# Optimization experiments

Measured on AMD Instinct MI355X. Metric: run time of the kernel, lower is better.

## Reference

```python
import jax, jax.numpy as jnp
import numpy as np
from jax import lax

DEPTH, DIM, HEADS, DHEAD = 4, 384, 8, 64
INNER = HEADS * DHEAD          # 512
HID = int(DIM * 0.25)          # 96 (hardcoded in Transformer_Conv)
B, Hg, Wg = 8, 32, 32
N = Hg * Wg
SCALE = DHEAD ** -0.5
EPS = 1e-5


def _layer_norm(x, w, b):
    mu = jnp.mean(x, axis=-1, keepdims=True)
    var = jnp.mean(jnp.square(x - mu), axis=-1, keepdims=True)
    return (x - mu) * lax.rsqrt(var + EPS) * w + b


def setup_inputs() -> dict:
    key = jax.random.key(0)
    ks = jax.random.split(key, 8)
    s = 0.02
    return {
        "x": jax.random.normal(ks[0], (B, N, DIM), jnp.float32),
        "ln1_w": jnp.ones((DEPTH, DIM), jnp.float32),
        "ln1_b": jnp.zeros((DEPTH, DIM), jnp.float32),
        "w_qkv": jax.random.normal(ks[1], (DEPTH, DIM, 3 * INNER), jnp.float32) * s,
        "w_out": jax.random.normal(ks[2], (DEPTH, INNER, DIM), jnp.float32) * s,
        "b_out": jnp.zeros((DEPTH, DIM), jnp.float32),
        "ln2_w": jnp.ones((DEPTH, DIM), jnp.float32),
        "ln2_b": jnp.zeros((DEPTH, DIM), jnp.float32),
        "fc1_w": jax.random.normal(ks[3], (DEPTH, DIM, HID), jnp.float32) * s,
        "fc1_b": jnp.zeros((DEPTH, HID), jnp.float32),
        "dw_w": jax.random.normal(ks[4], (DEPTH, HID, 1, 3, 3), jnp.float32) * s,
        "dw_b": jnp.zeros((DEPTH, HID), jnp.float32),
        "fc2_w": jax.random.normal(ks[5], (DEPTH, HID, DIM), jnp.float32) * s,
        "fc2_b": jnp.zeros((DEPTH, DIM), jnp.float32),
        "H": Hg,
        "W": Wg,
    }


def _forward(x, ln1_w, ln1_b, w_qkv, w_out, b_out, ln2_w, ln2_b,
             fc1_w, fc1_b, dw_w, dw_b, fc2_w, fc2_b, H, W):
    b, n, c = x.shape
    attn_last = None
    for l in range(DEPTH):
        # ---- PreNorm + Attention (with post-softmax cross-layer residual) ----
        xn = _layer_norm(x, ln1_w[l], ln1_b[l])
        qkv = xn @ w_qkv[l]                                   # [b, n, 3*inner]
        q, k, v = jnp.split(qkv, 3, axis=-1)
        q = q.reshape(b, n, HEADS, DHEAD).transpose(0, 2, 1, 3)  # bhnd
        k = k.reshape(b, n, HEADS, DHEAD).transpose(0, 2, 1, 3)
        v = v.reshape(b, n, HEADS, DHEAD).transpose(0, 2, 1, 3)
        dots = jnp.einsum("bhid,bhjd->bhij", q, k) * SCALE
        attn = jax.nn.softmax(dots, axis=-1)
        if attn_last is not None:
            attn = attn + attn_last
        attn_last = attn
        out = jnp.einsum("bhij,bhjd->bhid", attn, v)
        out = out.transpose(0, 2, 1, 3).reshape(b, n, INNER)
        x = out @ w_out[l] + b_out[l] + x
        # ---- ConvFFN: LN -> fc1 -> depthwise conv 3x3 -> GELU -> fc2 ----
        y = _layer_norm(x, ln2_w[l], ln2_b[l])
        y = y @ fc1_w[l] + fc1_b[l]                            # [b, n, HID]
        y4 = y.transpose(0, 2, 1).reshape(b, HID, H, W)
        y4 = lax.conv_general_dilated(
            y4, dw_w[l], window_strides=(1, 1), padding="SAME",
            feature_group_count=HID,
            dimension_numbers=("NCHW", "OIHW", "NCHW"),
        ) + dw_b[l][None, :, None, None]
        y = y4.reshape(b, HID, n).transpose(0, 2, 1)
        y = jax.nn.gelu(y, approximate=False)                  # torch nn.GELU (erf)
        x = y @ fc2_w[l] + fc2_b[l] + x
    return x


def reference(x, ln1_w, ln1_b, w_qkv, w_out, b_out, ln2_w, ln2_b,
              fc1_w, fc1_b, dw_w, dw_b, fc2_w, fc2_b, H, W):
    return _forward(x, ln1_w, ln1_b, w_qkv, w_out, b_out, ln2_w, ln2_b,
                    fc1_w, fc1_b, dw_w, dw_b, fc2_w, fc2_b, H, W)
```

## Files before the change

### kernel.cpp

```cpp
#include <hip/hip_runtime.h>
#include <hip/hip_bf16.h>
#include <math.h>

#define DEPTH 4
#define DIM 384
#define HEADS 8
#define DHEAD 64
#define INNER 512
#define HID 96
#define BATCH 8
#define NTOK 1024
#define ROWS (BATCH*NTOK)

typedef __attribute__((ext_vector_type(8))) _Float16 half8;
typedef __attribute__((ext_vector_type(4))) _Float16 half4;
typedef __attribute__((ext_vector_type(4))) float f32x4;

__global__ __launch_bounds__(256) void ln_kernel(const float* __restrict__ x,
                                                 const float* __restrict__ w,
                                                 const float* __restrict__ b,
                                                 _Float16* __restrict__ out) {
  const int row = blockIdx.x * 4 + (threadIdx.x >> 6);
  const int lane = threadIdx.x & 63;
  const float* xr = x + (size_t)row * DIM;
  float v[6];
  float s = 0.f;
#pragma unroll
  for (int i = 0; i < 6; ++i) {
    v[i] = xr[lane + i * 64];
    s += v[i];
  }
#pragma unroll
  for (int m = 1; m < 64; m <<= 1) s += __shfl_xor(s, m);
  const float mean = s * (1.0f / DIM);
  float sq = 0.f;
#pragma unroll
  for (int i = 0; i < 6; ++i) {
    v[i] -= mean;
    sq += v[i] * v[i];
  }
#pragma unroll
  for (int m = 1; m < 64; m <<= 1) sq += __shfl_xor(sq, m);
  const float rs = rsqrtf(sq * (1.0f / DIM) + 1e-5f);
  _Float16* orow = out + (size_t)row * DIM;
#pragma unroll
  for (int i = 0; i < 6; ++i)
    orow[lane + i * 64] = (_Float16)(v[i] * rs * w[lane + i * 64] + b[lane + i * 64]);
}

__global__ __launch_bounds__(256) void transposeW(const float* __restrict__ in0,
                                                  _Float16* __restrict__ out0,
                                                  int K, int N, int Npad) {
  __shared__ float t[32][33];
  const int l = blockIdx.z;
  const float* in = in0 + (size_t)l * K * N;
  _Float16* out = out0 + (size_t)l * Npad * K;
  const int k0 = blockIdx.x * 32, n0 = blockIdx.y * 32;
  const int tx = threadIdx.x & 31, ty = threadIdx.x >> 5;
#pragma unroll
  for (int i = 0; i < 4; ++i) {
    int k = k0 + ty + i * 8, n = n0 + tx;
    t[ty + i * 8][tx] = (k < K && n < N) ? in[(size_t)k * N + n] : 0.f;
  }
  __syncthreads();
#pragma unroll
  for (int i = 0; i < 4; ++i) {
    int n = n0 + ty + i * 8, k = k0 + tx;
    if (n < Npad && k < K) out[(size_t)n * K + k] = (_Float16)t[tx][ty + i * 8];
  }
}

template <bool BIAS, bool RES, bool OUT16, int KT, int NT>
__global__ __launch_bounds__(256) void hgemm(const _Float16* __restrict__ A,
                                             const _Float16* __restrict__ Bt,
                                             const float* __restrict__ bias,
                                             const float* __restrict__ res,
                                             void* __restrict__ Cout) {
  const int tid = threadIdx.x;
  const int wave = tid >> 6, lane = tid & 63;
  const int wm = wave >> 1, wn = wave & 1;
  const int g = lane >> 4, lr = lane & 15;
  const int m0 = blockIdx.x * 128 + wm * 64;
  const int n0 = blockIdx.y * 128 + wn * 64;
  f32x4 acc[4][4];
#pragma unroll
  for (int i = 0; i < 4; ++i)
#pragma unroll
    for (int j = 0; j < 4; ++j) acc[i][j] = {0.f, 0.f, 0.f, 0.f};

  const _Float16* Ap = A + (size_t)(m0 + lr) * KT + g * 8;
  const _Float16* Bp = Bt + (size_t)(n0 + lr) * KT + g * 8;
  for (int k0 = 0; k0 < KT; k0 += 32) {
    half8 af[4], bf[4];
#pragma unroll
    for (int i = 0; i < 4; ++i)
      af[i] = *(const half8*)(Ap + (size_t)i * 16 * KT + k0);
#pragma unroll
    for (int j = 0; j < 4; ++j)
      bf[j] = *(const half8*)(Bp + (size_t)j * 16 * KT + k0);
#pragma unroll
    for (int i = 0; i < 4; ++i)
#pragma unroll
      for (int j = 0; j < 4; ++j)
        acc[i][j] =
            __builtin_amdgcn_mfma_f32_16x16x32_f16(af[i], bf[j], acc[i][j], 0, 0, 0);
  }

#pragma unroll
  for (int i = 0; i < 4; ++i) {
#pragma unroll
    for (int j = 0; j < 4; ++j) {
      const int n = n0 + j * 16 + lr;
      if (NT % 128 == 0 || n < NT) {
        float bb = BIAS ? bias[n] : 0.f;
#pragma unroll
        for (int jj = 0; jj < 4; ++jj) {
          const int m = m0 + i * 16 + g * 4 + jj;
          float v = acc[i][j][jj] + bb;
          const size_t idx = (size_t)m * NT + n;
          if (RES) v += res[idx];
          if (OUT16)
            ((_Float16*)Cout)[idx] = (_Float16)v;
          else
            ((float*)Cout)[idx] = v;
        }
      }
    }
  }
}

__global__ __launch_bounds__(256) void hgemm_fc1(const _Float16* __restrict__ A,
                                                 const _Float16* __restrict__ Bt,
                                                 const float* __restrict__ bias,
                                                 _Float16* __restrict__ C) {
  const int tid = threadIdx.x;
  const int wave = tid >> 6, lane = tid & 63;
  const int g = lane >> 4, lr = lane & 15;
  const int m0 = blockIdx.x * 32;
  const int n0 = wave * 32;
  f32x4 acc[2][2];
#pragma unroll
  for (int i = 0; i < 2; ++i)
#pragma unroll
    for (int j = 0; j < 2; ++j) acc[i][j] = {0.f, 0.f, 0.f, 0.f};

  const _Float16* Ap = A + (size_t)(m0 + lr) * DIM + g * 8;
  const _Float16* Bp = Bt + (size_t)(n0 + lr) * DIM + g * 8;
  for (int k0 = 0; k0 < DIM; k0 += 32) {
    half8 af[2], bf[2];
#pragma unroll
    for (int i = 0; i < 2; ++i)
      af[i] = *(const half8*)(Ap + (size_t)i * 16 * DIM + k0);
#pragma unroll
    for (int j = 0; j < 2; ++j)
      bf[j] = *(const half8*)(Bp + (size_t)j * 16 * DIM + k0);
#pragma unroll
    for (int i = 0; i < 2; ++i)
#pragma unroll
      for (int j = 0; j < 2; ++j)
        acc[i][j] =
            __builtin_amdgcn_mfma_f32_16x16x32_f16(af[i], bf[j], acc[i][j], 0, 0, 0);
  }

#pragma unroll
  for (int i = 0; i < 2; ++i)
#pragma unroll
    for (int j = 0; j < 2; ++j) {
      const int n = n0 + j * 16 + lr;
      if (n < HID) {
        const float bb = bias[n];
#pragma unroll
        for (int jj = 0; jj < 4; ++jj) {
          const int m = m0 + i * 16 + g * 4 + jj;
          C[(size_t)m * HID + n] = (_Float16)(acc[i][j][jj] + bb);
        }
      }
    }
}

__global__ __launch_bounds__(256) void hgemm_qkv(const _Float16* __restrict__ A,
                                                 const _Float16* __restrict__ Bt,
                                                 _Float16* __restrict__ qh,
                                                 _Float16* __restrict__ kT,
                                                 _Float16* __restrict__ vTn) {
  const int tid = threadIdx.x;
  const int wave = tid >> 6, lane = tid & 63;
  const int wm = wave >> 1, wn = wave & 1;
  const int g = lane >> 4, lr = lane & 15;
  const int m0 = blockIdx.x * 128 + wm * 64;
  const int n0 = blockIdx.y * 128 + wn * 64;
  f32x4 acc[4][4];
#pragma unroll
  for (int i = 0; i < 4; ++i)
#pragma unroll
    for (int j = 0; j < 4; ++j) acc[i][j] = {0.f, 0.f, 0.f, 0.f};

  const _Float16* Ap = A + (size_t)(m0 + lr) * DIM + g * 8;
  const _Float16* Bp = Bt + (size_t)(n0 + lr) * DIM + g * 8;
  for (int k0 = 0; k0 < DIM; k0 += 32) {
    half8 af[4], bf[4];
#pragma unroll
    for (int i = 0; i < 4; ++i)
      af[i] = *(const half8*)(Ap + (size_t)i * 16 * DIM + k0);
#pragma unroll
    for (int j = 0; j < 4; ++j)
      bf[j] = *(const half8*)(Bp + (size_t)j * 16 * DIM + k0);
#pragma unroll
    for (int i = 0; i < 4; ++i)
#pragma unroll
      for (int j = 0; j < 4; ++j)
        acc[i][j] =
            __builtin_amdgcn_mfma_f32_16x16x32_f16(af[i], bf[j], acc[i][j], 0, 0, 0);
  }

  if (n0 < 512) {
#pragma unroll
    for (int i = 0; i < 4; ++i)
#pragma unroll
      for (int j = 0; j < 4; ++j) {
        const int n = n0 + j * 16 + lr;
#pragma unroll
        for (int jj = 0; jj < 4; ++jj) {
          const int m = m0 + i * 16 + g * 4 + jj;
          qh[(size_t)m * 512 + n] = (_Float16)acc[i][j][jj];
        }
      }
  } else if (n0 < 1024) {
#pragma unroll
    for (int j = 0; j < 4; ++j) {
      const int n = n0 + j * 16 + lr;
      const int hk = (n - 512) >> 6, d = (n - 512) & 63;
      const int sb = d >> 5, dd = d & 31;
#pragma unroll
      for (int i = 0; i < 4; ++i)
#pragma unroll
        for (int jj = 0; jj < 4; ++jj) {
          const int m = m0 + i * 16 + g * 4 + jj;
          const int bb = m >> 10, tok = m & 1023;
          const int f = tok >> 4, tr = tok & 15;
          kT[((((size_t)(bb * 8 + hk) * 64 + f) * 2 + sb) * 16 + tr) * 32 + dd] =
              (_Float16)acc[i][j][jj];
        }
    }
  } else {
    const int bb = m0 >> 10;
    const int tok0 = (m0 & 1023) + g * 4;
#pragma unroll
    for (int j = 0; j < 4; ++j) {
      const int dg = n0 + j * 16 + lr - 1024;
      const int hk = dg >> 6, d = dg & 63;
#pragma unroll
      for (int i = 0; i < 4; ++i) {
        const int tok = tok0 + i * 16;
        const int kb = tok >> 5, tk = tok & 31;
        half4 t = {(_Float16)acc[i][j][0], (_Float16)acc[i][j][1],
                   (_Float16)acc[i][j][2], (_Float16)acc[i][j][3]};
        *(half4*)(vTn + (((size_t)(bb * 8 + hk) * 32 + kb) * 64 + d) * 32 + tk) = t;
      }
    }
  }
}

__device__ __forceinline__ int pidx(int r, int c) {
  return ((((r << 11) + (c << 1)) ^ ((r & 15) << 4)) >> 1);
}

__global__ __launch_bounds__(512) void attn_kernel(
    const _Float16* __restrict__ qh, const _Float16* __restrict__ kT,
    const _Float16* __restrict__ vTn, _Float16* __restrict__ store,
    _Float16* __restrict__ aout, int has_prev, int write_store) {
  __shared__ __align__(16) char smem[32768];
  _Float16* P = (_Float16*)smem;
  float (*red)[16][68] = (float (*)[16][68])smem;
  __shared__ float partial[8][16];
  __shared__ float invs[16];

  const int tid = threadIdx.x;
  const int wave = tid >> 6, lane = tid & 63;
  const int g = lane >> 4, lr = lane & 15;
  const int blk = blockIdx.x;
  const int xcd = blk & 7, j0 = blk >> 3;
  const int bh = xcd * 8 + (j0 >> 6), rt = j0 & 63;
  const int b = bh >> 3, h = bh & 7;
  const int r0 = rt << 4;

  const _Float16* qbase = qh + ((size_t)b * NTOK + r0) * 512 + h * DHEAD;
  const _Float16* kbase = kT + (size_t)bh * 64 * 1024;
  const _Float16* vbase = vTn + (size_t)bh * 32 * 2048;
  const size_t gbase = ((size_t)bh * NTOK + r0) * 1024;

  half8 prev[4];
  if (has_prev) {
#pragma unroll
    for (int it = 0; it < 4; ++it) {
      const int e = tid + it * 512;
      const int r = e >> 7, c8 = (e & 127) << 3;
      prev[it] = *(const half8*)(store + gbase + ((size_t)r << 10) + c8);
    }
  }

  const half8 a0 = *(const half8*)(qbase + (size_t)lr * 512 + g * 8);
  const half8 a1 = *(const half8*)(qbase + (size_t)lr * 512 + 32 + g * 8);

  float p[8][4];
  float rs[4] = {0.f, 0.f, 0.f, 0.f};
  __builtin_amdgcn_s_setprio(1);
#pragma unroll
  for (int fl = 0; fl < 8; ++fl) {
    const int f = wave * 8 + fl;
    const _Float16* kb = kbase + (size_t)f * 1024 + lr * 32 + g * 8;
    half8 b0 = *(const half8*)(kb);
    half8 b1 = *(const half8*)(kb + 512);
    f32x4 acc = {0.f, 0.f, 0.f, 0.f};
    acc = __builtin_amdgcn_mfma_f32_16x16x32_f16(a0, b0, acc, 0, 0, 0);
    acc = __builtin_amdgcn_mfma_f32_16x16x32_f16(a1, b1, acc, 0, 0, 0);
#pragma unroll
    for (int j = 0; j < 4; ++j) {
      float e = __expf(acc[j] * 0.125f);
      p[fl][j] = e;
      rs[j] += e;
    }
  }
  __builtin_amdgcn_s_setprio(0);
#pragma unroll
  for (int j = 0; j < 4; ++j) {
    rs[j] += __shfl_xor(rs[j], 1);
    rs[j] += __shfl_xor(rs[j], 2);
    rs[j] += __shfl_xor(rs[j], 4);
    rs[j] += __shfl_xor(rs[j], 8);
  }
  if (lr == 0) {
#pragma unroll
    for (int j = 0; j < 4; ++j) partial[wave][g * 4 + j] = rs[j];
  }
  __syncthreads();
  if (tid < 16) {
    float s = 0.f;
#pragma unroll
    for (int w = 0; w < 8; ++w) s += partial[w][tid];
    invs[tid] = 1.0f / s;
  }
  __syncthreads();

#pragma unroll
  for (int fl = 0; fl < 8; ++fl) {
    const int c = wave * 128 + fl * 16 + lr;
#pragma unroll
    for (int j = 0; j < 4; ++j) {
      const int r = g * 4 + j;
      P[pidx(r, c)] = (_Float16)(p[fl][j] * invs[r]);
    }
  }
  __syncthreads();

#pragma unroll
  for (int it = 0; it < 4; ++it) {
    const int e = tid + it * 512;
    const int r = e >> 7, c8 = (e & 127) << 3;
    half8 pv = *(half8*)(P + pidx(r, c8));
    if (has_prev) {
#pragma unroll
      for (int k = 0; k < 8; ++k)
        pv[k] = (_Float16)((float)pv[k] + (float)prev[it][k]);
      *(half8*)(P + pidx(r, c8)) = pv;
    }
    if (write_store)
      *(half8*)(store + gbase + ((size_t)r << 10) + c8) = pv;
  }
  __syncthreads();

  const int nf = wave & 3, kh = wave >> 2;
  f32x4 oacc = {0.f, 0.f, 0.f, 0.f};
  __builtin_amdgcn_s_setprio(1);
#pragma unroll
  for (int ks = 0; ks < 16; ++ks) {
    const int kb = kh * 16 + ks;
    half8 af = *(half8*)(P + pidx(lr, kb * 32 + g * 8));
    half8 bfv = *(const half8*)(vbase + ((size_t)kb * 64 + nf * 16 + lr) * 32 + g * 8);
    oacc = __builtin_amdgcn_mfma_f32_16x16x32_f16(af, bfv, oacc, 0, 0, 0);
  }
  __builtin_amdgcn_s_setprio(0);
  __syncthreads();
#pragma unroll
  for (int j = 0; j < 4; ++j) red[kh][g * 4 + j][nf * 16 + lr] = oacc[j];
  __syncthreads();
#pragma unroll
  for (int it = 0; it < 2; ++it) {
    const int e = tid + it * 512;
    const int r = e >> 6, d = e & 63;
    float s = red[0][r][d] + red[1][r][d];
    aout[((size_t)b * NTOK + r0 + r) * INNER + h * DHEAD + d] = (_Float16)s;
  }
}

__global__ __launch_bounds__(256) void dwconv_gelu(const _Float16* __restrict__ y,
                                                   const float* __restrict__ w,
                                                   const float* __restrict__ bs,
                                                   _Float16* __restrict__ out) {
  const int blk = blockIdx.x;
  const int bb = blk / 96;
  const int rem = blk - bb * 96;
  const int hh = rem / 3, cg = rem - (rem / 3) * 3;
#pragma unroll
  for (int it = 0; it < 4; ++it) {
    const int e = threadIdx.x + it * 256;
    const int c = cg * 32 + (e & 31), ww = e >> 5;
    float acc = bs[c];
#pragma unroll
    for (int dh = 0; dh < 3; ++dh) {
      int ih = hh + dh - 1;
      if (ih < 0 || ih >= 32) continue;
#pragma unroll
      for (int dw = 0; dw < 3; ++dw) {
        int iw = ww + dw - 1;
        if (iw < 0 || iw >= 32) continue;
        acc += (float)y[((size_t)(bb * NTOK + ih * 32 + iw)) * HID + c] *
               w[c * 9 + dh * 3 + dw];
      }
    }
    float gl = 0.5f * acc * (1.f + erff(acc * 0.70710678118f));
    out[((size_t)(bb * NTOK + hh * 32 + ww)) * HID + c] = (_Float16)gl;
  }
}

extern "C" void kernel_launch(void* const* d_in, const int* in_sizes, int n_in,
                              void* d_out, int out_size, void* d_ws,
                              size_t ws_size, hipStream_t stream) {
  const float* x_in  = (const float*)d_in[0];
  const float* ln1_w = (const float*)d_in[1];
  const float* ln1_b = (const float*)d_in[2];
  const float* w_qkv = (const float*)d_in[3];
  const float* w_out = (const float*)d_in[4];
  const float* b_out = (const float*)d_in[5];
  const float* ln2_w = (const float*)d_in[6];
  const float* ln2_b = (const float*)d_in[7];
  const float* fc1_w = (const float*)d_in[8];
  const float* fc1_b = (const float*)d_in[9];
  const float* dw_w  = (const float*)d_in[10];
  const float* dw_b  = (const float*)d_in[11];
  const float* fc2_w = (const float*)d_in[12];
  const float* fc2_b = (const float*)d_in[13];

  float* x = (float*)d_out;

  char* ws = (char*)d_ws;
  _Float16* xn    = (_Float16*)ws; ws += (size_t)ROWS * DIM * 2;
  _Float16* qh    = (_Float16*)ws; ws += (size_t)ROWS * 512 * 2;
  _Float16* kT    = (_Float16*)ws; ws += (size_t)64 * 64 * 1024 * 2;
  _Float16* vTn   = (_Float16*)ws; ws += (size_t)64 * 32 * 2048 * 2;
  _Float16* aout  = (_Float16*)ws; ws += (size_t)ROWS * INNER * 2;
  _Float16* y1    = (_Float16*)ws; ws += (size_t)ROWS * HID * 2;
  _Float16* y2    = (_Float16*)ws; ws += (size_t)ROWS * HID * 2;
  _Float16* wqkvT = (_Float16*)ws; ws += (size_t)DEPTH * 1536 * DIM * 2;
  _Float16* woutT = (_Float16*)ws; ws += (size_t)DEPTH * DIM * INNER * 2;
  _Float16* fc1T  = (_Float16*)ws; ws += (size_t)DEPTH * 128 * DIM * 2;
  _Float16* fc2T  = (_Float16*)ws; ws += (size_t)DEPTH * DIM * HID * 2;
  _Float16* astore = (_Float16*)ws;

  transposeW<<<dim3(12, 48, DEPTH), 256, 0, stream>>>(w_qkv, wqkvT, DIM,
                                                      1536, 1536);
  transposeW<<<dim3(16, 12, DEPTH), 256, 0, stream>>>(w_out, woutT, INNER,
                                                      DIM, DIM);
  transposeW<<<dim3(12, 4, DEPTH), 256, 0, stream>>>(fc1_w, fc1T, DIM, HID,
                                                     128);
  transposeW<<<dim3(3, 12, DEPTH), 256, 0, stream>>>(fc2_w, fc2T, HID, DIM,
                                                     DIM);

  hipMemcpyAsync(x, x_in, (size_t)ROWS * DIM * 4, hipMemcpyDeviceToDevice,
                 stream);

  for (int l = 0; l < DEPTH; ++l) {
    ln_kernel<<<ROWS / 4, 256, 0, stream>>>(x, ln1_w + l * DIM,
                                            ln1_b + l * DIM, xn);
    hgemm_qkv<<<dim3(64, 12), 256, 0, stream>>>(
        xn, wqkvT + (size_t)l * 1536 * DIM, qh, kT, vTn);
    attn_kernel<<<4096, 512, 0, stream>>>(qh, kT, vTn, astore, aout,
                                          l > 0 ? 1 : 0,
                                          l < DEPTH - 1 ? 1 : 0);
    hgemm<true, true, false, INNER, DIM><<<dim3(64, 3), 256, 0, stream>>>(
        aout, woutT + (size_t)l * DIM * INNER, b_out + l * DIM, x, x);
    ln_kernel<<<ROWS / 4, 256, 0, stream>>>(x, ln2_w + l * DIM,
                                            ln2_b + l * DIM, xn);
    hgemm_fc1<<<ROWS / 32, 256, 0, stream>>>(
        xn, fc1T + (size_t)l * 128 * DIM, fc1_b + l * HID, y1);
    dwconv_gelu<<<768, 256, 0, stream>>>(y1, dw_w + l * HID * 9,
                                         dw_b + l * HID, y2);
    hgemm<true, true, false, HID, DIM><<<dim3(64, 3), 256, 0, stream>>>(
        y2, fc2T + (size_t)l * DIM * HID, fc2_b + l * DIM, x, x);
  }
}
```

Baseline: 792.3 us.

## Store GEMM operands in 16x32 fragment-tiled layout for contiguous MFMA loads

Activations (LN output, Q, attention output, dwconv output) and transposed weights are now written in a fragment-blocked layout: 16 rows by 32 k-columns stored contiguously. Each wave's half8 MFMA operand load then reads one contiguous 1 KB block instead of 16 strided rows, which improves coalescing in the GEMMs that read global memory directly. The attention kernel also holds the summed probabilities in registers and writes the cross-layer attention store after the PV MFMA loop, taking that write off the critical path. In exchange, the producer kernels do scattered stores with more complex index math.

```diff
diff --git a/kernel.cpp b/kernel.cpp
--- a/kernel.cpp
+++ b/kernel.cpp
@@ -16,10 +16,11 @@
 typedef __attribute__((ext_vector_type(4))) _Float16 half4;
 typedef __attribute__((ext_vector_type(4))) float f32x4;
 
+
 __global__ __launch_bounds__(256) void ln_kernel(const float* __restrict__ x,
                                                  const float* __restrict__ w,
                                                  const float* __restrict__ b,
-                                                 _Float16* __restrict__ out) {
+                                                 _Float16* __restrict__ outF) {
   const int row = blockIdx.x * 4 + (threadIdx.x >> 6);
   const int lane = threadIdx.x & 63;
   const float* xr = x + (size_t)row * DIM;
@@ -42,10 +43,13 @@
 #pragma unroll
   for (int m = 1; m < 64; m <<= 1) sq += __shfl_xor(sq, m);
   const float rs = rsqrtf(sq * (1.0f / DIM) + 1e-5f);
-  _Float16* orow = out + (size_t)row * DIM;
-#pragma unroll
-  for (int i = 0; i < 6; ++i)
-    orow[lane + i * 64] = (_Float16)(v[i] * rs * w[lane + i * 64] + b[lane + i * 64]);
+  const int f = row >> 4, lr = row & 15;
+#pragma unroll
+  for (int i = 0; i < 6; ++i) {
+    const int k = lane + i * 64;
+    outF[(((size_t)f * 12 + (k >> 5)) * 16 + lr) * 32 + (k & 31)] =
+        (_Float16)(v[i] * rs * w[k] + b[k]);
+  }
 }
 
 __global__ __launch_bounds__(256) void transposeW(const float* __restrict__ in0,
@@ -53,6 +57,7 @@
                                                   int K, int N, int Npad) {
   __shared__ float t[32][33];
   const int l = blockIdx.z;
+  const int KS = K >> 5;
   const float* in = in0 + (size_t)l * K * N;
   _Float16* out = out0 + (size_t)l * Npad * K;
   const int k0 = blockIdx.x * 32, n0 = blockIdx.y * 32;
@@ -60,44 +65,48 @@
 #pragma unroll
   for (int i = 0; i < 4; ++i) {
     int k = k0 + ty + i * 8, n = n0 + tx;
-    t[ty + i * 8][tx] = (k < K && n < N) ? in[(size_t)k * N + n] : 0.f;
-  }
-  __syncthreads();
+    t[ty + i * 8][tx] = (n < N) ? in[(size_t)k * N + n] : 0.f;
+  }
+  __syncthreads();
+  const int k = k0 + tx;
 #pragma unroll
   for (int i = 0; i < 4; ++i) {
-    int n = n0 + ty + i * 8, k = k0 + tx;
-    if (n < Npad && k < K) out[(size_t)n * K + k] = (_Float16)t[tx][ty + i * 8];
+    int n = n0 + ty + i * 8;
+    if (n < Npad)
+      out[(((size_t)(n >> 4) * KS + (k >> 5)) * 16 + (n & 15)) * 32 + (k & 31)] =
+          (_Float16)t[tx][ty + i * 8];
   }
 }
 
 template <bool BIAS, bool RES, bool OUT16, int KT, int NT>
-__global__ __launch_bounds__(256) void hgemm(const _Float16* __restrict__ A,
-                                             const _Float16* __restrict__ Bt,
+__global__ __launch_bounds__(256) void hgemm(const _Float16* __restrict__ AF,
+                                             const _Float16* __restrict__ BF,
                                              const float* __restrict__ bias,
                                              const float* __restrict__ res,
                                              void* __restrict__ Cout) {
+  constexpr int KS = KT / 32;
   const int tid = threadIdx.x;
   const int wave = tid >> 6, lane = tid & 63;
   const int wm = wave >> 1, wn = wave & 1;
   const int g = lane >> 4, lr = lane & 15;
   const int m0 = blockIdx.x * 128 + wm * 64;
   const int n0 = blockIdx.y * 128 + wn * 64;
+  const int fA = m0 >> 4, fB = n0 >> 4;
+  const int lo = lr * 32 + g * 8;
   f32x4 acc[4][4];
 #pragma unroll
   for (int i = 0; i < 4; ++i)
 #pragma unroll
     for (int j = 0; j < 4; ++j) acc[i][j] = {0.f, 0.f, 0.f, 0.f};
 
-  const _Float16* Ap = A + (size_t)(m0 + lr) * KT + g * 8;
-  const _Float16* Bp = Bt + (size_t)(n0 + lr) * KT + g * 8;
-  for (int k0 = 0; k0 < KT; k0 += 32) {
+  for (int ks = 0; ks < KS; ++ks) {
     half8 af[4], bf[4];
 #pragma unroll
     for (int i = 0; i < 4; ++i)
-      af[i] = *(const half8*)(Ap + (size_t)i * 16 * KT + k0);
+      af[i] = *(const half8*)(AF + ((size_t)(fA + i) * KS + ks) * 512 + lo);
 #pragma unroll
     for (int j = 0; j < 4; ++j)
-      bf[j] = *(const half8*)(Bp + (size_t)j * 16 * KT + k0);
+      bf[j] = *(const half8*)(BF + ((size_t)(fB + j) * KS + ks) * 512 + lo);
 #pragma unroll
     for (int i = 0; i < 4; ++i)
 #pragma unroll
@@ -129,31 +138,30 @@
   }
 }
 
-__global__ __launch_bounds__(256) void hgemm_fc1(const _Float16* __restrict__ A,
-                                                 const _Float16* __restrict__ Bt,
+__global__ __launch_bounds__(256) void hgemm_fc1(const _Float16* __restrict__ AF,
+                                                 const _Float16* __restrict__ BF,
                                                  const float* __restrict__ bias,
                                                  _Float16* __restrict__ C) {
   const int tid = threadIdx.x;
   const int wave = tid >> 6, lane = tid & 63;
   const int g = lane >> 4, lr = lane & 15;
   const int m0 = blockIdx.x * 32;
-  const int n0 = wave * 32;
+  const int fA = m0 >> 4, fB = wave * 2;
+  const int lo = lr * 32 + g * 8;
   f32x4 acc[2][2];
 #pragma unroll
   for (int i = 0; i < 2; ++i)
 #pragma unroll
     for (int j = 0; j < 2; ++j) acc[i][j] = {0.f, 0.f, 0.f, 0.f};
 
-  const _Float16* Ap = A + (size_t)(m0 + lr) * DIM + g * 8;
-  const _Float16* Bp = Bt + (size_t)(n0 + lr) * DIM + g * 8;
-  for (int k0 = 0; k0 < DIM; k0 += 32) {
+  for (int ks = 0; ks < 12; ++ks) {
     half8 af[2], bf[2];
 #pragma unroll
     for (int i = 0; i < 2; ++i)
-      af[i] = *(const half8*)(Ap + (size_t)i * 16 * DIM + k0);
+      af[i] = *(const half8*)(AF + ((size_t)(fA + i) * 12 + ks) * 512 + lo);
 #pragma unroll
     for (int j = 0; j < 2; ++j)
-      bf[j] = *(const half8*)(Bp + (size_t)j * 16 * DIM + k0);
+      bf[j] = *(const half8*)(BF + ((size_t)(fB + j) * 12 + ks) * 512 + lo);
 #pragma unroll
     for (int i = 0; i < 2; ++i)
 #pragma unroll
@@ -166,7 +174,7 @@
   for (int i = 0; i < 2; ++i)
 #pragma unroll
     for (int j = 0; j < 2; ++j) {
-      const int n = n0 + j * 16 + lr;
+      const int n = wave * 32 + j * 16 + lr;
       if (n < HID) {
         const float bb = bias[n];
 #pragma unroll
@@ -178,9 +186,9 @@
     }
 }
 
-__global__ __launch_bounds__(256) void hgemm_qkv(const _Float16* __restrict__ A,
-                                                 const _Float16* __restrict__ Bt,
-                                                 _Float16* __restrict__ qh,
+__global__ __launch_bounds__(256) void hgemm_qkv(const _Float16* __restrict__ AF,
+                                                 const _Float16* __restrict__ BF,
+                                                 _Float16* __restrict__ qF,
                                                  _Float16* __restrict__ kT,
                                                  _Float16* __restrict__ vTn) {
   const int tid = threadIdx.x;
@@ -189,22 +197,22 @@
   const int g = lane >> 4, lr = lane & 15;
   const int m0 = blockIdx.x * 128 + wm * 64;
   const int n0 = blockIdx.y * 128 + wn * 64;
+  const int fA = m0 >> 4, fB = n0 >> 4;
+  const int lo = lr * 32 + g * 8;
   f32x4 acc[4][4];
 #pragma unroll
   for (int i = 0; i < 4; ++i)
 #pragma unroll
     for (int j = 0; j < 4; ++j) acc[i][j] = {0.f, 0.f, 0.f, 0.f};
 
-  const _Float16* Ap = A + (size_t)(m0 + lr) * DIM + g * 8;
-  const _Float16* Bp = Bt + (size_t)(n0 + lr) * DIM + g * 8;
-  for (int k0 = 0; k0 < DIM; k0 += 32) {
+  for (int ks = 0; ks < 12; ++ks) {
     half8 af[4], bf[4];
 #pragma unroll
     for (int i = 0; i < 4; ++i)
-      af[i] = *(const half8*)(Ap + (size_t)i * 16 * DIM + k0);
+      af[i] = *(const half8*)(AF + ((size_t)(fA + i) * 12 + ks) * 512 + lo);
 #pragma unroll
     for (int j = 0; j < 4; ++j)
-      bf[j] = *(const half8*)(Bp + (size_t)j * 16 * DIM + k0);
+      bf[j] = *(const half8*)(BF + ((size_t)(fB + j) * 12 + ks) * 512 + lo);
 #pragma unroll
     for (int i = 0; i < 4; ++i)
 #pragma unroll
@@ -222,7 +230,8 @@
 #pragma unroll
         for (int jj = 0; jj < 4; ++jj) {
           const int m = m0 + i * 16 + g * 4 + jj;
-          qh[(size_t)m * 512 + n] = (_Float16)acc[i][j][jj];
+          qF[(((size_t)(m >> 4) * 16 + (n >> 5)) * 16 + (m & 15)) * 32 + (n & 31)] =
+              (_Float16)acc[i][j][jj];
         }
       }
   } else if (n0 < 1024) {
@@ -266,9 +275,9 @@
 }
 
 __global__ __launch_bounds__(512) void attn_kernel(
-    const _Float16* __restrict__ qh, const _Float16* __restrict__ kT,
+    const _Float16* __restrict__ qF, const _Float16* __restrict__ kT,
     const _Float16* __restrict__ vTn, _Float16* __restrict__ store,
-    _Float16* __restrict__ aout, int has_prev, int write_store) {
+    _Float16* __restrict__ aoutF, int has_prev, int write_store) {
   __shared__ __align__(16) char smem[32768];
   _Float16* P = (_Float16*)smem;
   float (*red)[16][68] = (float (*)[16][68])smem;
@@ -283,8 +292,8 @@
   const int bh = xcd * 8 + (j0 >> 6), rt = j0 & 63;
   const int b = bh >> 3, h = bh & 7;
   const int r0 = rt << 4;
-
-  const _Float16* qbase = qh + ((size_t)b * NTOK + r0) * 512 + h * DHEAD;
+  const int fq = (b * NTOK + r0) >> 4;
+
   const _Float16* kbase = kT + (size_t)bh * 64 * 1024;
   const _Float16* vbase = vTn + (size_t)bh * 32 * 2048;
   const size_t gbase = ((size_t)bh * NTOK + r0) * 1024;
@@ -299,8 +308,10 @@
     }
   }
 
-  const half8 a0 = *(const half8*)(qbase + (size_t)lr * 512 + g * 8);
-  const half8 a1 = *(const half8*)(qbase + (size_t)lr * 512 + 32 + g * 8);
+  const half8 a0 =
+      *(const half8*)(qF + (((size_t)fq * 16 + h * 2) * 16 + lr) * 32 + g * 8);
+  const half8 a1 = *(const half8*)(
+      qF + (((size_t)fq * 16 + h * 2 + 1) * 16 + lr) * 32 + g * 8);
 
   float p[8][4];
   float rs[4] = {0.f, 0.f, 0.f, 0.f};
@@ -353,6 +364,7 @@
   }
   __syncthreads();
 
+  half8 pvreg[4];
 #pragma unroll
   for (int it = 0; it < 4; ++it) {
     const int e = tid + it * 512;
@@ -364,8 +376,7 @@
         pv[k] = (_Float16)((float)pv[k] + (float)prev[it][k]);
       *(half8*)(P + pidx(r, c8)) = pv;
     }
-    if (write_store)
-      *(half8*)(store + gbase + ((size_t)r << 10) + c8) = pv;
+    pvreg[it] = pv;
   }
   __syncthreads();
 
@@ -381,6 +392,16 @@
   }
   __builtin_amdgcn_s_setprio(0);
   __syncthreads();
+
+  if (write_store) {
+#pragma unroll
+    for (int it = 0; it < 4; ++it) {
+      const int e = tid + it * 512;
+      const int r = e >> 7, c8 = (e & 127) << 3;
+      *(half8*)(store + gbase + ((size_t)r << 10) + c8) = pvreg[it];
+    }
+  }
+
 #pragma unroll
   for (int j = 0; j < 4; ++j) red[kh][g * 4 + j][nf * 16 + lr] = oacc[j];
   __syncthreads();
@@ -389,14 +410,15 @@
     const int e = tid + it * 512;
     const int r = e >> 6, d = e & 63;
     float s = red[0][r][d] + red[1][r][d];
-    aout[((size_t)b * NTOK + r0 + r) * INNER + h * DHEAD + d] = (_Float16)s;
+    aoutF[(((size_t)fq * 16 + h * 2 + (d >> 5)) * 16 + r) * 32 + (d & 31)] =
+        (_Float16)s;
   }
 }
 
 __global__ __launch_bounds__(256) void dwconv_gelu(const _Float16* __restrict__ y,
                                                    const float* __restrict__ w,
                                                    const float* __restrict__ bs,
-                                                   _Float16* __restrict__ out) {
+                                                   _Float16* __restrict__ outF) {
   const int blk = blockIdx.x;
   const int bb = blk / 96;
   const int rem = blk - bb * 96;
@@ -419,7 +441,8 @@
       }
     }
     float gl = 0.5f * acc * (1.f + erff(acc * 0.70710678118f));
-    out[((size_t)(bb * NTOK + hh * 32 + ww)) * HID + c] = (_Float16)gl;
+    const int f = bb * 64 + hh * 2 + (ww >> 4);
+    outF[(((size_t)f * 3 + cg) * 16 + (ww & 15)) * 32 + (e & 31)] = (_Float16)gl;
   }
 }
 
@@ -444,13 +467,13 @@
   float* x = (float*)d_out;
 
   char* ws = (char*)d_ws;
-  _Float16* xn    = (_Float16*)ws; ws += (size_t)ROWS * DIM * 2;
-  _Float16* qh    = (_Float16*)ws; ws += (size_t)ROWS * 512 * 2;
+  _Float16* xnF   = (_Float16*)ws; ws += (size_t)ROWS * DIM * 2;
+  _Float16* qF    = (_Float16*)ws; ws += (size_t)ROWS * 512 * 2;
   _Float16* kT    = (_Float16*)ws; ws += (size_t)64 * 64 * 1024 * 2;
   _Float16* vTn   = (_Float16*)ws; ws += (size_t)64 * 32 * 2048 * 2;
-  _Float16* aout  = (_Float16*)ws; ws += (size_t)ROWS * INNER * 2;
+  _Float16* aoutF = (_Float16*)ws; ws += (size_t)ROWS * INNER * 2;
   _Float16* y1    = (_Float16*)ws; ws += (size_t)ROWS * HID * 2;
-  _Float16* y2    = (_Float16*)ws; ws += (size_t)ROWS * HID * 2;
+  _Float16* y2F   = (_Float16*)ws; ws += (size_t)ROWS * HID * 2;
   _Float16* wqkvT = (_Float16*)ws; ws += (size_t)DEPTH * 1536 * DIM * 2;
   _Float16* woutT = (_Float16*)ws; ws += (size_t)DEPTH * DIM * INNER * 2;
   _Float16* fc1T  = (_Float16*)ws; ws += (size_t)DEPTH * 128 * DIM * 2;
@@ -471,21 +494,21 @@
 
   for (int l = 0; l < DEPTH; ++l) {
     ln_kernel<<<ROWS / 4, 256, 0, stream>>>(x, ln1_w + l * DIM,
-                                            ln1_b + l * DIM, xn);
+                                            ln1_b + l * DIM, xnF);
     hgemm_qkv<<<dim3(64, 12), 256, 0, stream>>>(
-        xn, wqkvT + (size_t)l * 1536 * DIM, qh, kT, vTn);
-    attn_kernel<<<4096, 512, 0, stream>>>(qh, kT, vTn, astore, aout,
+        xnF, wqkvT + (size_t)l * 1536 * DIM, qF, kT, vTn);
+    attn_kernel<<<4096, 512, 0, stream>>>(qF, kT, vTn, astore, aoutF,
                                           l > 0 ? 1 : 0,
                                           l < DEPTH - 1 ? 1 : 0);
     hgemm<true, true, false, INNER, DIM><<<dim3(64, 3), 256, 0, stream>>>(
-        aout, woutT + (size_t)l * DIM * INNER, b_out + l * DIM, x, x);
+        aoutF, woutT + (size_t)l * DIM * INNER, b_out + l * DIM, x, x);
     ln_kernel<<<ROWS / 4, 256, 0, stream>>>(x, ln2_w + l * DIM,
-                                            ln2_b + l * DIM, xn);
+                                            ln2_b + l * DIM, xnF);
     hgemm_fc1<<<ROWS / 32, 256, 0, stream>>>(
-        xn, fc1T + (size_t)l * 128 * DIM, fc1_b + l * HID, y1);
+        xnF, fc1T + (size_t)l * 128 * DIM, fc1_b + l * HID, y1);
     dwconv_gelu<<<768, 256, 0, stream>>>(y1, dw_w + l * HID * 9,
-                                         dw_b + l * HID, y2);
+                                         dw_b + l * HID, y2F);
     hgemm<true, true, false, HID, DIM><<<dim3(64, 3), 256, 0, stream>>>(
-        y2, fc2T + (size_t)l * DIM * HID, fc2_b + l * DIM, x, x);
-  }
-}
+        y2F, fc2T + (size_t)l * DIM * HID, fc2_b + l * DIM, x, x);
+  }
+}
```

New measurement: 650.4 us (median of 2 runs). 1.22x faster.
